# Optimization experiments

Measured on AMD Instinct MI355X. Metric: run time of the kernel, lower is better.

The kernel has to match this reference:

```python
import jax, jax.numpy as jnp
import numpy as np


def _sin_rpe(Lq, d_model, dtype):
    # sinusoidal relative-position embeddings for positions -(Lq-1)..(Lq-1)
    inv_freq = 1.0 / (10000.0 ** (jnp.arange(0, d_model, 2, dtype=jnp.float32) / d_model))
    pos = jnp.arange(-(Lq - 1), Lq, dtype=jnp.float32)  # [2Lq-1]
    ang = pos[:, None] * inv_freq[None, :]               # [2Lq-1, d_model/2]
    emb = jnp.zeros((2 * Lq - 1, d_model), dtype=jnp.float32)
    emb = emb.at[:, 0::2].set(jnp.sin(ang)).at[:, 1::2].set(jnp.cos(ang))
    return emb.astype(dtype)


def _rel_shift(x):
    # Transformer-XL relative shift. x: [B,H,Lq,Lr] with Lr = 2Lq-1
    B, H, Lq, Lr = x.shape
    xp = jnp.concatenate([jnp.zeros((B, H, Lq, 1), x.dtype), x], axis=-1)
    xp = xp.reshape(B, H, Lr + 1, Lq)
    return xp[:, :, 1:].reshape(B, H, Lq, Lr)[..., Lr - Lq:]


def setup_inputs() -> dict:
    key = jax.random.key(0)
    ks = jax.random.split(key, 7)
    B, Lq, D, H = 1, 2048, 1024, 16
    d_head = D // H
    s = 0.02
    return {
        "w": jax.random.normal(ks[0], (B, Lq, D), jnp.float32),
        "Wq": jax.random.normal(ks[1], (D, D), jnp.float32) * s,
        "Wk": jax.random.normal(ks[2], (D, D), jnp.float32) * s,
        "Wv": jax.random.normal(ks[3], (D, D), jnp.float32) * s,
        "Wr": jax.random.normal(ks[4], (D, D), jnp.float32) * s,
        "u_bias": jax.random.normal(ks[5], (H, d_head), jnp.float32) * 0.02,
        "v_bias": jax.random.normal(ks[6], (H, d_head), jnp.float32) * 0.02,
    }


def reference(w, Wq, Wk, Wv, Wr, u_bias, v_bias):
    B, Lq, D = w.shape
    H, d_head = u_bias.shape
    scale = 1.0 / np.sqrt(d_head).astype(np.float32)
    r = _sin_rpe(Lq, D, w.dtype)                          # [2Lq-1, D]
    # torch Linear: y = x @ W.T
    q = (w @ Wq.T).reshape(B, Lq, H, d_head).transpose(0, 2, 1, 3)  # [B,H,Lq,d]
    k = (w @ Wk.T).reshape(B, Lq, H, d_head).transpose(0, 2, 1, 3)
    v = (w @ Wv.T).reshape(B, Lq, H, d_head).transpose(0, 2, 1, 3)
    rp = (r @ Wr.T).reshape(2 * Lq - 1, H, d_head).transpose(1, 0, 2)  # [H,2Lq-1,d]
    AC = jnp.einsum('bhid,bhjd->bhij', q + u_bias[None, :, None, :], k)   # [B,H,Lq,Lq]
    BD = jnp.einsum('bhid,hjd->bhij', q + v_bias[None, :, None, :], rp)   # [B,H,Lq,2Lq-1]
    BD = _rel_shift(BD)                                                   # [B,H,Lq,Lq]
    attn = jax.nn.softmax((AC + BD) * scale, axis=-1)
    out = jnp.einsum('bhij,bhjd->bhid', attn, v)          # [B,H,Lq,d]
    return out.transpose(0, 2, 1, 3).reshape(B, Lq, D)
```

## Files before the change

kernel.cpp:

```cpp
#include <hip/hip_runtime.h>
#include <math.h>
#include <stddef.h>

#define LQ 2048
#define DM 1024
#define NH 16
#define DH 64
#define LR 4095

typedef __attribute__((ext_vector_type(4))) float f4v;
typedef __attribute__((ext_vector_type(8))) short s8v;
typedef __attribute__((ext_vector_type(2))) unsigned short us2;
typedef __attribute__((ext_vector_type(8))) unsigned short us8;
typedef __attribute__((ext_vector_type(2))) unsigned int u32x2;
typedef __attribute__((ext_vector_type(4))) unsigned int u32x4;

__device__ __forceinline__ unsigned short f2bf(float x) {
    unsigned int u = __float_as_uint(x);
    return (unsigned short)((u + 0x7FFFu + ((u >> 16) & 1u)) >> 16);
}
__device__ __forceinline__ float bf2f(unsigned short s) {
    return __uint_as_float(((unsigned int)s) << 16);
}
__device__ __forceinline__ unsigned cvtpk(float lo, float hi) {
    unsigned r;
    asm("v_cvt_pk_bf16_f32 %0, %1, %2" : "=v"(r) : "v"(lo), "v"(hi));
    return r;
}
template<int CTRL>
__device__ __forceinline__ float rot16(float x) {
    return __uint_as_float((unsigned)__builtin_amdgcn_update_dpp(
        0, (int)__float_as_uint(x), CTRL, 0xF, 0xF, false));
}
#define GLOAD16(g, l) __builtin_amdgcn_global_load_lds((g), (l), 16, 0, 0)
#define WAVE_LDS_FENCE() do { \
    asm volatile("s_waitcnt lgkmcnt(0)" ::: "memory"); \
    __builtin_amdgcn_sched_barrier(0); } while (0)

#define MFMA16(a, b, c) __builtin_amdgcn_mfma_f32_16x16x32_bf16((a), (b), (c), 0, 0, 0)

__device__ __forceinline__ s8v sw_read8(const unsigned short* base, int row, int colshort) {
    int byte = (row * 128 + colshort * 2) ^ ((row & 7) << 4);
    return *(const s8v*)((const char*)base + byte);
}

__global__ __launch_bounds__(256)
void prep(const float* __restrict__ w, const float* __restrict__ Wq,
          const float* __restrict__ Wk, const float* __restrict__ Wv,
          const float* __restrict__ Wr, unsigned short* __restrict__ dst,
          unsigned short* __restrict__ r, unsigned short* __restrict__ rpg) {
    int b = blockIdx.x;
    if (b < 3072) {
        size_t e0 = ((size_t)b * 256 + threadIdx.x) * 8;
        const float* src;
        if (e0 < (size_t)LQ * DM) src = w + e0;
        else {
            size_t ro = e0 - (size_t)LQ * DM;
            int wi = (int)(ro >> 20);
            size_t off = ro & 1048575;
            src = (wi == 0 ? Wq : wi == 1 ? Wk : wi == 2 ? Wv : Wr) + off;
        }
        f4v a = *(const f4v*)src;
        f4v c = *(const f4v*)(src + 4);
        us8 o;
        o[0]=f2bf(a[0]); o[1]=f2bf(a[1]); o[2]=f2bf(a[2]); o[3]=f2bf(a[3]);
        o[4]=f2bf(c[0]); o[5]=f2bf(c[1]); o[6]=f2bf(c[2]); o[7]=f2bf(c[3]);
        *(us8*)(dst + e0) = o;
    } else if (b < 11262) {
        int tg = (b - 3072) * 256 + threadIdx.x;
        int gm = tg >> 9, c2 = tg & 511;
        float invf = expf(-(float)c2 * (9.210340371976184f / 512.0f));
        float ang = (float)(gm - (LQ - 1)) * invf;
        us2 o; o[0] = f2bf(sinf(ang)); o[1] = f2bf(cosf(ang));
        *(us2*)&r[(size_t)gm * DM + c2 * 2] = o;
    } else {
        int idx = (b - 11262) * 2048 + threadIdx.x * 8;
        unsigned short* p = (idx < 131072)
            ? (rpg - 131072 + idx)
            : (rpg + (size_t)LR * DM + (idx - 131072));
        *(us8*)p = (us8){0,0,0,0,0,0,0,0};
    }
}

__global__ __launch_bounds__(256)
void proj_all(const unsigned short* __restrict__ wbf, const unsigned short* __restrict__ rr,
              const unsigned short* __restrict__ Wqb, const unsigned short* __restrict__ Wkb,
              const unsigned short* __restrict__ Wvb, const unsigned short* __restrict__ Wrb,
              unsigned short* __restrict__ qb, unsigned short* __restrict__ kkb,
              unsigned short* __restrict__ vtg, unsigned short* __restrict__ rpg) {
    __shared__ unsigned short As[128 * 64];
    __shared__ unsigned short Bs[128 * 64];
    int bid = blockIdx.x;
    int mat, mblk, nblk;
    if (bid < 384) { mat = bid >> 7; int rm = bid & 127; mblk = rm >> 3; nblk = rm & 7; }
    else           { mat = 3; int rm = bid - 384; mblk = rm >> 3; nblk = rm & 7; }
    const int M = (mat < 3) ? LQ : LR;
    const unsigned short* A = (mat < 3) ? wbf : rr;
    const unsigned short* B = mat == 0 ? Wqb : mat == 1 ? Wkb : mat == 2 ? Wvb : Wrb;
    unsigned short* C = mat == 0 ? qb : mat == 1 ? kkb : mat == 2 ? vtg : rpg;
    const int m0 = mblk * 128, n0 = nblk * 128;
    const int t = threadIdx.x;
    const int w = t >> 6, lan16 = t & 15, lgrp = (t & 63) >> 4;
    const int wm = (w >> 1) * 64, wn = (w & 1) * 64;
    f4v acc[4][4] = {};

    for (int k0 = 0; k0 < DM; k0 += 64) {
        #pragma unroll
        for (int it = 0; it < 4; ++it) {
            int slot = it * 256 + t;
            int row = slot >> 3, c8 = slot & 7;
            int gm = m0 + row; if (gm > M - 1) gm = M - 1;
            GLOAD16(A + (size_t)gm * DM + k0 + c8 * 8,
                    (char*)As + (size_t)(it * 256 + (t & ~63)) * 16);
            GLOAD16(B + (size_t)(n0 + row) * DM + k0 + c8 * 8,
                    (char*)Bs + (size_t)(it * 256 + (t & ~63)) * 16);
        }
        __syncthreads();
        #pragma unroll
        for (int kk = 0; kk < 2; ++kk) {
            s8v aF[4], bF[4];
            #pragma unroll
            for (int i = 0; i < 4; ++i) {
                aF[i] = *(const s8v*)&As[(wm + i * 16 + lan16) * 64 + kk * 32 + lgrp * 8];
                bF[i] = *(const s8v*)&Bs[(wn + i * 16 + lan16) * 64 + kk * 32 + lgrp * 8];
            }
            #pragma unroll
            for (int i = 0; i < 4; ++i)
                #pragma unroll
                for (int j = 0; j < 4; ++j)
                    acc[i][j] = MFMA16(aF[i], bF[j], acc[i][j]);
        }
        __syncthreads();
    }
    if (mat != 2) {
        #pragma unroll
        for (int i = 0; i < 4; ++i)
            #pragma unroll
            for (int j = 0; j < 4; ++j)
                #pragma unroll
                for (int rg = 0; rg < 4; ++rg) {
                    int row = m0 + wm + i * 16 + lgrp * 4 + rg;
                    if (row < M)
                        C[(size_t)row * DM + n0 + wn + j * 16 + lan16] = f2bf(acc[i][j][rg]);
                }
    } else {
        #pragma unroll
        for (int i = 0; i < 4; ++i)
            #pragma unroll
            for (int j = 0; j < 4; ++j) {
                int n = n0 + wn + j * 16 + lan16;
                int m = m0 + wm + i * 16 + lgrp * 4;
                u32x2 pp;
                pp[0] = cvtpk(acc[i][j][0], acc[i][j][1]);
                pp[1] = cvtpk(acc[i][j][2], acc[i][j][3]);
                *(u32x2*)&C[(size_t)n * LQ + m] = pp;
            }
    }
}

__global__ __launch_bounds__(256, 2)
void attn_mfma(const unsigned short* __restrict__ q, const unsigned short* __restrict__ kkg,
               const unsigned short* __restrict__ vtg, const unsigned short* __restrict__ rpg,
               const float* __restrict__ ub, const float* __restrict__ vb,
               float* __restrict__ Oa, float* __restrict__ Ob,
               float* __restrict__ la, float* __restrict__ lb) {
    __shared__ unsigned short Kb[2][64 * 64];
    __shared__ unsigned short Bb[2][128 * 64];
    __shared__ unsigned short Vb[64 * 64];
    __shared__ unsigned short Gtw[4][80 * 20];
    __shared__ unsigned short Pt[4][64 * 18];

    const int dd = blockIdx.x;
    const int f = (dd & 7) * 128 + (dd >> 3);
    const int h = f >> 6;
    const int sp = (f >> 5) & 1;
    const int i0 = (f & 31) * 64;
    const int col0 = h * DH;
    float* Op = sp ? Ob : Oa;
    float* lp = sp ? lb : la;
    const int jbeg = sp * 1024;

    const int t = threadIdx.x;
    const int w = t >> 6, lan16 = t & 15, lgrp = (t & 63) >> 4;
    const int W = w * 16;
    const int cbase = 48 - W;
    const float C1 = 0.125f * 1.4426950408889634f;
    const float C0 = -4.0f * 1.4426950408889634f;

    unsigned short* gw = Gtw[w];
    unsigned short* pw = Pt[w];

    union uv { u32x4 u; s8v s; };
    auto mkfrag = [&](int gi, const float* bias, s8v* dstf) {
        #pragma unroll
        for (int kk = 0; kk < 2; ++kk) {
            int cb = kk * 32 + lgrp * 8;
            us8 qv = (us8){0,0,0,0,0,0,0,0};
            if (gi < LQ) qv = *(const us8*)(q + (size_t)gi * DM + col0 + cb);
            f4v b0 = *(const f4v*)(bias + col0 + cb);
            f4v b1 = *(const f4v*)(bias + col0 + cb + 4);
            uv o;
            o.u[0] = cvtpk(bf2f(qv[0]) + b0[0], bf2f(qv[1]) + b0[1]);
            o.u[1] = cvtpk(bf2f(qv[2]) + b0[2], bf2f(qv[3]) + b0[3]);
            o.u[2] = cvtpk(bf2f(qv[4]) + b1[0], bf2f(qv[5]) + b1[1]);
            o.u[3] = cvtpk(bf2f(qv[6]) + b1[2], bf2f(qv[7]) + b1[3]);
            dstf[kk] = o.s;
        }
    };
    s8v quF[2], qvlF[2], qvsF[2];
    mkfrag(i0 + W + lan16, ub, quF);
    mkfrag(i0 + W + lan16, vb, qvlF);
    mkfrag(i0 + W + 1 + lan16, vb, qvsF);

    auto stageK = [&](int j0, int buf) {
        #pragma unroll
        for (int it = 0; it < 2; ++it) {
            int slot = it * 256 + t;
            int row = slot >> 3, c8 = (t & 7) ^ (row & 7);
            GLOAD16(kkg + (size_t)(j0 + row) * DM + col0 + c8 * 8,
                    (char*)&Kb[buf][0] + (size_t)(it * 256 + (t & ~63)) * 16);
        }
    };
    auto stageB = [&](int rel, int buf) {
        int base = (rel <= 0) ? rel + 4031 : rel - 65;
        #pragma unroll
        for (int it = 0; it < 4; ++it) {
            int slot = it * 256 + t;
            int row = slot >> 3, c8 = (t & 7) ^ (row & 7);
            GLOAD16(rpg + (ptrdiff_t)(base + row) * DM + col0 + c8 * 8,
                    (char*)&Bb[buf][0] + (size_t)(it * 256 + (t & ~63)) * 16);
        }
    };
    auto stageV = [&](int j0) {
        #pragma unroll
        for (int it = 0; it < 2; ++it) {
            int slot = it * 256 + t;
            int row = slot >> 3, c8 = (t & 7) ^ (row & 7);
            GLOAD16(vtg + (size_t)(col0 + row) * LQ + j0 + c8 * 8,
                    (char*)&Vb[0] + (size_t)(it * 256 + (t & ~63)) * 16);
        }
    };

    f4v accO[4] = {};
    float lsum[4] = {0.f, 0.f, 0.f, 0.f};

    stageK(jbeg, 0);
    stageB(jbeg - i0, 0);

    auto tile_body = [&](int tt, int cur) {
        const int j0 = jbeg + tt * 64;
        const int rel = j0 - i0;
        stageV(j0);
        const int tn = (tt < 15) ? tt + 1 : 15;
        stageK(jbeg + tn * 64, cur ^ 1);
        stageB(jbeg + tn * 64 - i0, cur ^ 1);
        __builtin_amdgcn_sched_barrier(0);
        asm volatile("s_waitcnt vmcnt(8)" ::: "memory");
        __builtin_amdgcn_s_barrier();
        __builtin_amdgcn_sched_barrier(0);

        __builtin_amdgcn_s_setprio(1);
        f4v acF[4] = {};
        #pragma unroll
        for (int nf = 0; nf < 4; ++nf)
            #pragma unroll
            for (int kk = 0; kk < 2; ++kk) {
                s8v bF = sw_read8(&Kb[cur][0], nf * 16 + lan16, kk * 32 + lgrp * 8);
                acF[nf] = MFMA16(quF[kk], bF, acF[nf]);
            }
        f4v g[5] = {};
        {
            const s8v* qf = (rel <= 0) ? qvlF : qvsF;
            #pragma unroll
            for (int c = 0; c < 5; ++c)
                #pragma unroll
                for (int kk = 0; kk < 2; ++kk) {
                    s8v bF = sw_read8(&Bb[cur][0], cbase + c * 16 + lan16, kk * 32 + lgrp * 8);
                    g[c] = MFMA16(qf[kk], bF, g[c]);
                }
        }
        __builtin_amdgcn_s_setprio(0);
        if (rel == 0) {
            #pragma unroll
            for (int c = 0; c < 5; ++c) {
                int trow = -65 + cbase + c * 16 + lan16;
                const unsigned short* bp = rpg + (ptrdiff_t)trow * DM + col0;
                #pragma unroll
                for (int kk = 0; kk < 2; ++kk) {
                    us8 bv = *(const us8*)(bp + kk * 32 + lgrp * 8);
                    g[c] = MFMA16(qvsF[kk], (s8v)bv, g[c]);
                }
            }
        }
        #pragma unroll
        for (int c = 0; c < 5; ++c) {
            int cl = c * 16 + lan16;
            u32x2 pp;
            pp[0] = cvtpk(g[c][0], g[c][1]);
            pp[1] = cvtpk(g[c][2], g[c][3]);
            *(u32x2*)&gw[cl * 20 + lgrp * 4] = pp;
        }
        WAVE_LDS_FENCE();

        #pragma unroll
        for (int nf = 0; nf < 4; ++nf) {
            int jl = nf * 16 + lan16;
            float pp[4];
            #pragma unroll
            for (int rg = 0; rg < 4; ++rg) {
                const int rhat = lgrp * 4 + rg;
                float bd = bf2f(gw[(jl - rhat + 15) * 20 + rhat]);
                pp[rg] = exp2f(fmaf(acF[nf][rg] + bd, C1, C0));
                lsum[rg] += pp[rg];
            }
            *(unsigned*)&pw[jl * 18 + lgrp * 4]     = cvtpk(pp[0], pp[1]);
            *(unsigned*)&pw[jl * 18 + lgrp * 4 + 2] = cvtpk(pp[2], pp[3]);
        }
        WAVE_LDS_FENCE();

        s8v pF[2];
        #pragma unroll
        for (int kk = 0; kk < 2; ++kk) {
            us8 tmp;
            #pragma unroll
            for (int e = 0; e < 8; ++e)
                tmp[e] = pw[(kk * 32 + lgrp * 8 + e) * 18 + lan16];
            pF[kk] = (s8v)tmp;
        }
        __builtin_amdgcn_sched_barrier(0);
        asm volatile("s_waitcnt vmcnt(6)" ::: "memory");
        __builtin_amdgcn_s_barrier();
        __builtin_amdgcn_sched_barrier(0);

        __builtin_amdgcn_s_setprio(1);
        #pragma unroll
        for (int nf = 0; nf < 4; ++nf)
            #pragma unroll
            for (int kk = 0; kk < 2; ++kk) {
                s8v vF = sw_read8(&Vb[0], nf * 16 + lan16, kk * 32 + lgrp * 8);
                accO[nf] = MFMA16(pF[kk], vF, accO[nf]);
            }
        __builtin_amdgcn_s_setprio(0);
        __builtin_amdgcn_sched_barrier(0);
        __builtin_amdgcn_s_barrier();
        __builtin_amdgcn_sched_barrier(0);
    };

    #pragma unroll 1
    for (int tp = 0; tp < 8; ++tp) {
        tile_body(tp * 2, 0);
        tile_body(tp * 2 + 1, 1);
    }

    #pragma unroll
    for (int rg = 0; rg < 4; ++rg) {
        float s = lsum[rg];
        s += rot16<0x121>(s);
        s += rot16<0x122>(s);
        s += rot16<0x124>(s);
        s += rot16<0x128>(s);
        const int row = i0 + W + lgrp * 4 + rg;
        if (lan16 == 0) lp[h * LQ + row] = s;
        #pragma unroll
        for (int nf = 0; nf < 4; ++nf)
            Op[(size_t)row * DM + col0 + nf * 16 + lan16] = accO[nf][rg];
    }
}

__global__ __launch_bounds__(256)
void combine(const float* __restrict__ Oa, const float* __restrict__ Ob,
             const float* __restrict__ la, const float* __restrict__ lb,
             float* __restrict__ out) {
    int i = blockIdx.x * 256 + threadIdx.x;
    int e0 = i * 4;
    int row = e0 >> 10;
    int h = (e0 & 1023) >> 6;
    float inv = 1.f / (la[h * LQ + row] + lb[h * LQ + row]);
    f4v a = *(const f4v*)(Oa + e0);
    f4v b = *(const f4v*)(Ob + e0);
    f4v o = (a + b) * inv;
    *(f4v*)(out + e0) = o;
}

extern "C" void kernel_launch(void* const* d_in, const int* in_sizes, int n_in,
                              void* d_out, int out_size, void* d_ws, size_t ws_size,
                              hipStream_t stream) {
    const float* w  = (const float*)d_in[0];
    const float* Wq = (const float*)d_in[1];
    const float* Wk = (const float*)d_in[2];
    const float* Wv = (const float*)d_in[3];
    const float* Wr = (const float*)d_in[4];
    const float* ub = (const float*)d_in[5];
    const float* vb = (const float*)d_in[6];
    float* out = (float*)d_out;

    const size_t U = 1048576;
    unsigned short* ws = (unsigned short*)d_ws;
    unsigned short* wbf = ws;
    unsigned short* Wqb = ws + 2 * U;
    unsigned short* Wkb = ws + 3 * U;
    unsigned short* Wvb = ws + 4 * U;
    unsigned short* Wrb = ws + 5 * U;
    unsigned short* qb  = ws + 6 * U;
    unsigned short* kkb = ws + 8 * U;
    unsigned short* vtg = ws + 10 * U;
    unsigned short* rpg = ws + 12 * U + 131072;
    unsigned short* r   = rpg + (size_t)LR * DM + 131072;

    float* Oa = (float*)r;
    float* Ob = (float*)ws;
    float* la = (float*)(ws + 4 * U);
    float* lb = la + NH * LQ;

    dim3 blk(256);
    hipLaunchKernelGGL(prep, dim3(11390), blk, 0, stream, w, Wq, Wk, Wv, Wr, wbf, r, rpg);
    hipLaunchKernelGGL(proj_all, dim3(640), blk, 0, stream,
                       wbf, r, Wqb, Wkb, Wvb, Wrb, qb, kkb, vtg, rpg);
    hipLaunchKernelGGL(attn_mfma, dim3(1024), blk, 0, stream,
                       qb, kkb, vtg, rpg, ub, vb, Oa, Ob, la, lb);
    hipLaunchKernelGGL(combine, dim3(2048), blk, 0, stream, Oa, Ob, la, lb, out);
}
```

Measured before the change: 139.4 us.

## Drop key-split attention and combine kernel; stage transposed V store through LDS

```diff
diff --git a/kernel.cpp b/kernel.cpp
--- a/kernel.cpp
+++ b/kernel.cpp
@@ -88,8 +88,9 @@
               const unsigned short* __restrict__ Wvb, const unsigned short* __restrict__ Wrb,
               unsigned short* __restrict__ qb, unsigned short* __restrict__ kkb,
               unsigned short* __restrict__ vtg, unsigned short* __restrict__ rpg) {
-    __shared__ unsigned short As[128 * 64];
-    __shared__ unsigned short Bs[128 * 64];
+    __shared__ unsigned short ldsbuf[2 * 128 * 64];
+    unsigned short* As = ldsbuf;
+    unsigned short* Bs = ldsbuf + 128 * 64;
     int bid = blockIdx.x;
     int mat, mblk, nblk;
     if (bid < 384) { mat = bid >> 7; int rm = bid & 127; mblk = rm >> 3; nblk = rm & 7; }
@@ -144,17 +145,28 @@
                         C[(size_t)row * DM + n0 + wn + j * 16 + lan16] = f2bf(acc[i][j][rg]);
                 }
     } else {
+        unsigned short* Ct = ldsbuf;
         #pragma unroll
         for (int i = 0; i < 4; ++i)
             #pragma unroll
             for (int j = 0; j < 4; ++j) {
-                int n = n0 + wn + j * 16 + lan16;
-                int m = m0 + wm + i * 16 + lgrp * 4;
+                int n = wn + j * 16 + lan16;
+                int mb = wm + i * 16 + lgrp * 4;
+                int byte = (n * 256 + mb * 2) ^ ((n & 7) << 4);
                 u32x2 pp;
                 pp[0] = cvtpk(acc[i][j][0], acc[i][j][1]);
                 pp[1] = cvtpk(acc[i][j][2], acc[i][j][3]);
-                *(u32x2*)&C[(size_t)n * LQ + m] = pp;
-            }
+                *(u32x2*)((char*)Ct + byte) = pp;
+            }
+        __syncthreads();
+        #pragma unroll
+        for (int it = 0; it < 8; ++it) {
+            int slot = it * 256 + t;
+            int n = slot >> 4, c8 = slot & 15;
+            int byte = (n * 256 + c8 * 16) ^ ((n & 7) << 4);
+            us8 v = *(const us8*)((const char*)Ct + byte);
+            *(us8*)&C[(size_t)(n0 + n) * LQ + m0 + c8 * 8] = v;
+        }
     }
 }
 
@@ -162,8 +174,7 @@
 void attn_mfma(const unsigned short* __restrict__ q, const unsigned short* __restrict__ kkg,
                const unsigned short* __restrict__ vtg, const unsigned short* __restrict__ rpg,
                const float* __restrict__ ub, const float* __restrict__ vb,
-               float* __restrict__ Oa, float* __restrict__ Ob,
-               float* __restrict__ la, float* __restrict__ lb) {
+               float* __restrict__ out) {
     __shared__ unsigned short Kb[2][64 * 64];
     __shared__ unsigned short Bb[2][128 * 64];
     __shared__ unsigned short Vb[64 * 64];
@@ -171,14 +182,10 @@
     __shared__ unsigned short Pt[4][64 * 18];
 
     const int dd = blockIdx.x;
-    const int f = (dd & 7) * 128 + (dd >> 3);
-    const int h = f >> 6;
-    const int sp = (f >> 5) & 1;
+    const int f = (dd & 7) * 64 + (dd >> 3);
+    const int h = f >> 5;
     const int i0 = (f & 31) * 64;
     const int col0 = h * DH;
-    float* Op = sp ? Ob : Oa;
-    float* lp = sp ? lb : la;
-    const int jbeg = sp * 1024;
 
     const int t = threadIdx.x;
     const int w = t >> 6, lan16 = t & 15, lgrp = (t & 63) >> 4;
@@ -244,16 +251,16 @@
     f4v accO[4] = {};
     float lsum[4] = {0.f, 0.f, 0.f, 0.f};
 
-    stageK(jbeg, 0);
-    stageB(jbeg - i0, 0);
+    stageK(0, 0);
+    stageB(0 - i0, 0);
 
     auto tile_body = [&](int tt, int cur) {
-        const int j0 = jbeg + tt * 64;
+        const int j0 = tt * 64;
         const int rel = j0 - i0;
         stageV(j0);
-        const int tn = (tt < 15) ? tt + 1 : 15;
-        stageK(jbeg + tn * 64, cur ^ 1);
-        stageB(jbeg + tn * 64 - i0, cur ^ 1);
+        const int tn = (tt < 31) ? tt + 1 : 31;
+        stageK(tn * 64, cur ^ 1);
+        stageB(tn * 64 - i0, cur ^ 1);
         __builtin_amdgcn_sched_barrier(0);
         asm volatile("s_waitcnt vmcnt(8)" ::: "memory");
         __builtin_amdgcn_s_barrier();
@@ -347,7 +354,7 @@
     };
 
     #pragma unroll 1
-    for (int tp = 0; tp < 8; ++tp) {
+    for (int tp = 0; tp < 16; ++tp) {
         tile_body(tp * 2, 0);
         tile_body(tp * 2 + 1, 1);
     }
@@ -359,27 +366,12 @@
         s += rot16<0x122>(s);
         s += rot16<0x124>(s);
         s += rot16<0x128>(s);
+        float inv = 1.f / s;
         const int row = i0 + W + lgrp * 4 + rg;
-        if (lan16 == 0) lp[h * LQ + row] = s;
         #pragma unroll
         for (int nf = 0; nf < 4; ++nf)
-            Op[(size_t)row * DM + col0 + nf * 16 + lan16] = accO[nf][rg];
+            out[(size_t)row * DM + col0 + nf * 16 + lan16] = accO[nf][rg] * inv;
     }
-}
-
-__global__ __launch_bounds__(256)
-void combine(const float* __restrict__ Oa, const float* __restrict__ Ob,
-             const float* __restrict__ la, const float* __restrict__ lb,
-             float* __restrict__ out) {
-    int i = blockIdx.x * 256 + threadIdx.x;
-    int e0 = i * 4;
-    int row = e0 >> 10;
-    int h = (e0 & 1023) >> 6;
-    float inv = 1.f / (la[h * LQ + row] + lb[h * LQ + row]);
-    f4v a = *(const f4v*)(Oa + e0);
-    f4v b = *(const f4v*)(Ob + e0);
-    f4v o = (a + b) * inv;
-    *(f4v*)(out + e0) = o;
 }
 
 extern "C" void kernel_launch(void* const* d_in, const int* in_sizes, int n_in,
@@ -407,16 +399,10 @@
     unsigned short* rpg = ws + 12 * U + 131072;
     unsigned short* r   = rpg + (size_t)LR * DM + 131072;
 
-    float* Oa = (float*)r;
-    float* Ob = (float*)ws;
-    float* la = (float*)(ws + 4 * U);
-    float* lb = la + NH * LQ;
-
     dim3 blk(256);
     hipLaunchKernelGGL(prep, dim3(11390), blk, 0, stream, w, Wq, Wk, Wv, Wr, wbf, r, rpg);
     hipLaunchKernelGGL(proj_all, dim3(640), blk, 0, stream,
                        wbf, r, Wqb, Wkb, Wvb, Wrb, qb, kkb, vtg, rpg);
-    hipLaunchKernelGGL(attn_mfma, dim3(1024), blk, 0, stream,
-                       qb, kkb, vtg, rpg, ub, vb, Oa, Ob, la, lb);
-    hipLaunchKernelGGL(combine, dim3(2048), blk, 0, stream, Oa, Ob, la, lb, out);
-}
+    hipLaunchKernelGGL(attn_mfma, dim3(512), blk, 0, stream,
+                       qb, kkb, vtg, rpg, ub, vb, out);
+}
```

Result: faster. 130.9 us (-6.1%).
